# Kernel tuning notes

Measured on AMD Instinct MI355X. Metric: run time of the kernel, lower is better.

The kernel has to match this reference:

```python
import jax, jax.numpy as jnp
import numpy as np

B, S = 16384, 2048
EPS = 1e-8


def _autocorr(x, lag):
    # Pearson correlation between x[:, :-lag] and x[:, lag:] (ddof cancels).
    a = x[:, :-lag]
    b = x[:, lag:]
    am = a.mean(axis=1, keepdims=True)
    bm = b.mean(axis=1, keepdims=True)
    cov = ((a - am) * (b - bm)).mean(axis=1)
    return cov / (a.std(axis=1) * b.std(axis=1))


def _stat_features(x):
    S_len = x.shape[1]
    mean = x.mean(axis=1)
    xc = x - mean[:, None]
    m2 = (xc ** 2).mean(axis=1)
    m3 = (xc ** 3).mean(axis=1)
    m4 = (xc ** 4).mean(axis=1)
    std = jnp.sqrt(m2)
    min_v = x.min(axis=1)
    max_v = x.max(axis=1)
    q = jnp.percentile(x, jnp.array([25.0, 50.0, 75.0]), axis=1)  # [3, B]
    p25, median, p75 = q[0], q[1], q[2]
    diff = jnp.diff(x, axis=1)
    std_diff = diff.std(axis=1)
    trend = std_diff / (std + EPS)
    ac1 = _autocorr(x, 1)
    ac7 = _autocorr(x, 7)
    ac24 = _autocorr(x, 24)
    cv = std / (jnp.abs(mean) + EPS)
    iqr = p75 - p25
    seasonal = x[:, ::24].var(axis=1) / (m2 + EPS)
    skew = m3 / (m2 ** 1.5)          # scipy.stats.skew, bias=True
    kurt = m4 / (m2 ** 2) - 3.0      # scipy.stats.kurtosis, Fisher, bias=True
    length = jnp.full_like(mean, float(S_len))
    sum_abs_diff = jnp.abs(diff).sum(axis=1)
    mean_abs_diff = jnp.abs(diff).mean(axis=1)
    feats = jnp.stack([mean, std, min_v, max_v, median, trend, ac1, ac7, ac24,
                       cv, iqr, seasonal, skew, kurt, length,
                       sum_abs_diff, mean_abs_diff, std_diff, p25, p75], axis=1)
    return jnp.where(jnp.isfinite(feats), feats, 0.0)


def setup_inputs() -> dict:
    key = jax.random.key(0)
    k0, k1, k2, k3, k4 = jax.random.split(key, 5)
    x = jax.random.normal(k0, (B, S), dtype=jnp.float32)
    W1 = jax.random.normal(k1, (64, 20), dtype=jnp.float32) * 0.1
    b1 = jnp.zeros((64,), dtype=jnp.float32)
    W2 = jax.random.normal(k3, (128, 64), dtype=jnp.float32) * 0.1
    b2 = jnp.zeros((128,), dtype=jnp.float32)
    return {"x": x, "W1": W1, "b1": b1, "W2": W2, "b2": b2}


def reference(x, W1, b1, W2, b2):
    feats = _stat_features(x)                      # [B, 20]
    h = jax.nn.relu(feats @ W1.T + b1)             # [B, 64] (dropout inactive at eval)
    return h @ W2.T + b2                           # [B, 128]
```

## Files before the change

kernel.cpp:

```cpp
#include <hip/hip_runtime.h>
#include <cmath>

constexpr int S_LEN = 2048;
constexpr float EPS = 1e-8f;

typedef unsigned uvec32 __attribute__((ext_vector_type(32)));

__device__ __forceinline__ float fin(float v) { return isfinite(v) ? v : 0.0f; }

__device__ __forceinline__ unsigned f2o_bits(unsigned u) {
    return (u & 0x80000000u) ? ~u : (u | 0x80000000u);
}
__device__ __forceinline__ float o2f(unsigned u) {
    return __uint_as_float((u & 0x80000000u) ? (u ^ 0x80000000u) : ~u);
}

template <int Ctrl, int Rmask>
__device__ __forceinline__ int dpp_zero_i(int x) {
    return __builtin_amdgcn_update_dpp(0, x, Ctrl, Rmask, 0xF, true);
}
template <int Ctrl>
__device__ __forceinline__ int dpp_keep_i(int x) {
    return __builtin_amdgcn_update_dpp(x, x, Ctrl, 0xF, 0xF, false);
}
__device__ __forceinline__ int wred_add_i(int v) {
    v += dpp_zero_i<0xB1, 0xF>(v);
    v += dpp_zero_i<0x4E, 0xF>(v);
    v += dpp_zero_i<0x114, 0xF>(v);
    v += dpp_zero_i<0x118, 0xF>(v);
    v += dpp_zero_i<0x142, 0xA>(v);
    v += dpp_zero_i<0x143, 0xC>(v);
    return __builtin_amdgcn_readlane(v, 63);
}
__device__ __forceinline__ float wred_add_f(float v) {
    #define ADDF(CT, RM) v += __uint_as_float((unsigned)dpp_zero_i<CT, RM>((int)__float_as_uint(v)))
    ADDF(0xB1, 0xF); ADDF(0x4E, 0xF); ADDF(0x114, 0xF);
    ADDF(0x118, 0xF); ADDF(0x142, 0xA); ADDF(0x143, 0xC);
    #undef ADDF
    return __uint_as_float((unsigned)__builtin_amdgcn_readlane((int)__float_as_uint(v), 63));
}
__device__ __forceinline__ float wred_min_f(float v) {
    #define MINF(CT) v = fminf(v, __uint_as_float((unsigned)dpp_keep_i<CT>((int)__float_as_uint(v))))
    MINF(0xB1); MINF(0x4E); MINF(0x114); MINF(0x118); MINF(0x142); MINF(0x143);
    #undef MINF
    return __uint_as_float((unsigned)__builtin_amdgcn_readlane((int)__float_as_uint(v), 63));
}
__device__ __forceinline__ float wred_max_f(float v) {
    #define MAXF(CT) v = fmaxf(v, __uint_as_float((unsigned)dpp_keep_i<CT>((int)__float_as_uint(v))))
    MAXF(0xB1); MAXF(0x4E); MAXF(0x114); MAXF(0x118); MAXF(0x142); MAXF(0x143);
    #undef MAXF
    return __uint_as_float((unsigned)__builtin_amdgcn_readlane((int)__float_as_uint(v), 63));
}
__device__ __forceinline__ unsigned wred_umin(unsigned v) {
    #define MINU(CT) { unsigned t = (unsigned)dpp_keep_i<CT>((int)v); v = v < t ? v : t; }
    MINU(0xB1) MINU(0x4E) MINU(0x114) MINU(0x118) MINU(0x142) MINU(0x143)
    #undef MINU
    return (unsigned)__builtin_amdgcn_readlane((int)v, 63);
}
__device__ __forceinline__ float readlane_f(float x, int l) {
    return __uint_as_float((unsigned)__builtin_amdgcn_readlane((int)__float_as_uint(x), l));
}

__device__ __forceinline__ void transpose32(uvec32& A) {
    #pragma unroll
    for (int j = 16; j; j >>= 1) {
        unsigned m = (j == 16) ? 0x0000FFFFu : (j == 8) ? 0x00FF00FFu
                   : (j == 4) ? 0x0F0F0F0Fu : (j == 2) ? 0x33333333u : 0x55555555u;
        #pragma unroll
        for (int k = 0; k < 32; k++) {
            if (!(k & j)) {
                unsigned t = (A[k] ^ (A[k | j] >> j)) & m;
                A[k] = A[k] ^ t;
                A[k | j] = A[k | j] ^ (t << j);
            }
        }
    }
}

#define VF(e) __uint_as_float(a[e])


__global__ __launch_bounds__(256) void statspct_kernel(
    const float* __restrict__ x, float* __restrict__ feats, int nrows)
{
    const int gw   = (blockIdx.x * 256 + threadIdx.x) >> 6;
    const int lane = threadIdx.x & 63;
    if (gw >= nrows) return;

    uvec32 a;
    const float* xr = x + (size_t)gw * S_LEN + lane * 32;
    #pragma unroll
    for (int q = 0; q < 8; q++) {
        float4 t = reinterpret_cast<const float4*>(xr)[q];
        a[4 * q + 0] = __float_as_uint(t.x); a[4 * q + 1] = __float_as_uint(t.y);
        a[4 * q + 2] = __float_as_uint(t.z); a[4 * q + 3] = __float_as_uint(t.w);
    }

    float s1 = 0.f, s2 = 0.f, sd2 = 0.f, sad = 0.f;
    float p1 = 0.f, p7 = 0.f, p24 = 0.f, se1 = 0.f, se2 = 0.f;
    float mn = VF(0), mx = VF(0);
    #pragma unroll
    for (int e = 0; e < 32; e++) {
        float val = VF(e);
        s1 += val; s2 = fmaf(val, val, s2);
        mn = fminf(mn, val); mx = fmaxf(mx, val);
    }
    #pragma unroll
    for (int e = 0; e < 31; e++) {
        float d = VF(e + 1) - VF(e);
        sd2 = fmaf(d, d, sd2); sad += fabsf(d);
        p1 = fmaf(VF(e), VF(e + 1), p1);
    }
    #pragma unroll
    for (int e = 0; e < 25; e++) p7 = fmaf(VF(e), VF(e + 7), p7);
    #pragma unroll
    for (int e = 0; e < 8; e++)  p24 = fmaf(VF(e), VF(e + 24), p24);

    const bool notlast = (lane < 63);
    #pragma unroll
    for (int j = 0; j < 24; j++) {
        float nb = __shfl_down(VF(j), 1, 64);
        float g = notlast ? nb : 0.f;
        p24 = fmaf(VF(8 + j), g, p24);
        if (j < 7) p7 = fmaf(VF(25 + j), g, p7);
        if (j == 0 && notlast) {
            float d = nb - VF(31);
            sd2 = fmaf(d, d, sd2); sad += fabsf(d);
            p1 = fmaf(VF(31), nb, p1);
        }
    }
    {
        int r3 = lane % 3;
        float sv = (r3 == 0) ? VF(0) : ((r3 == 1) ? VF(16) : VF(8));
        se1 += sv; se2 = fmaf(sv, sv, se2);
        if (r3 == 0) { se1 += VF(24); se2 = fmaf(VF(24), VF(24), se2); }
    }
    float aa = 0, bb = 0, h7v = 0, hq7v = 0;
    #pragma unroll
    for (int e = 0; e < 24; e++) {
        aa += VF(e); bb = fmaf(VF(e), VF(e), bb);
        if (e == 6) { h7v = aa; hq7v = bb; }
    }
    float cc = 0, dd = 0, t7v = 0, tq7v = 0;
    #pragma unroll
    for (int e = 31; e >= 8; e--) {
        cc += VF(e); dd = fmaf(VF(e), VF(e), dd);
        if (e == 25) { t7v = cc; tq7v = dd; }
    }
    const float h1  = readlane_f(VF(0), 0),   t1  = readlane_f(VF(31), 63);
    const float h7  = readlane_f(h7v, 0),     hq7 = readlane_f(hq7v, 0);
    const float h24 = readlane_f(aa, 0),      hq24 = readlane_f(bb, 0);
    const float t7  = readlane_f(t7v, 63),    tq7 = readlane_f(tq7v, 63);
    const float t24 = readlane_f(cc, 63),     tq24 = readlane_f(dd, 63);
    const float hq1 = h1 * h1, tq1 = t1 * t1;

    float S1  = wred_add_f(s1);
    float mean = S1 * (1.0f / S_LEN);
    float S2  = wred_add_f(s2);
    float SD2 = wred_add_f(sd2);
    float SAD = wred_add_f(sad);
    float P1  = wred_add_f(p1);
    float P7  = wred_add_f(p7);
    float P24 = wred_add_f(p24);
    float SE1 = wred_add_f(se1);
    float SE2 = wred_add_f(se2);
    float MN  = wred_min_f(mn);
    float MX  = wred_max_f(mx);

    float c2 = 0.f, c3 = 0.f, c4 = 0.f;
    #pragma unroll
    for (int e = 0; e < 32; e++) {
        float xc = VF(e) - mean;
        float q = xc * xc;
        c2 += q; c3 = fmaf(q, xc, c3); c4 = fmaf(q, q, c4);
    }
    float C2 = wred_add_f(c2), C3 = wred_add_f(c3), C4 = wred_add_f(c4);

    {
        const float Sf = (float)S_LEN;
        const float nd = Sf - 1.0f;
        float m2v = C2 / Sf, m3v = C3 / Sf, m4v = C4 / Sf;
        float stdv = sqrtf(m2v);
        float dmean = (t1 - h1) / nd;
        float dvar = SD2 / nd - dmean * dmean;
        float std_diff = sqrtf(fmaxf(dvar, 0.f));
        float trend = std_diff / (stdv + EPS);
        float ac[3];
        const float Ls[3] = {1.f, 7.f, 24.f};
        const float Ps[3] = {P1, P7, P24};
        const float hd[3] = {h1, h7, h24},   hqv[3] = {hq1, hq7, hq24};
        const float tl[3] = {t1, t7, t24},   tqv[3] = {tq1, tq7, tq24};
        #pragma unroll
        for (int q = 0; q < 3; q++) {
            float n = Sf - Ls[q];
            float sa = S1 - tl[q], sb = S1 - hd[q];
            float qa = S2 - tqv[q], qb = S2 - hqv[q];
            float am = sa / n, bm = sb / n;
            float cov = Ps[q] / n - am * bm;
            float as_ = sqrtf(fmaxf(qa / n - am * am, 0.f));
            float bs_ = sqrtf(fmaxf(qb / n - bm * bm, 0.f));
            ac[q] = cov / (as_ * bs_);
        }
        float cv = stdv / (fabsf(mean) + EPS);
        float sm = SE1 / 86.f;
        float svar = SE2 / 86.f - sm * sm;
        float seasonal = svar / (m2v + EPS);
        float skew = m3v / (m2v * stdv);
        float kurt = m4v / (m2v * m2v) - 3.f;
        if (lane == 0) {
            float4* fp = (float4*)(feats + (size_t)gw * 20);
            fp[0] = make_float4(fin(mean), fin(stdv), fin(MN), fin(MX));
            fp[1] = make_float4(fin(trend), fin(ac[0]), fin(ac[1]), fin(ac[2]));
            fp[2] = make_float4(fin(cv), fin(seasonal), fin(skew), fin(kurt));
            fp[3] = make_float4(Sf, fin(SAD), fin(SAD / nd), fin(std_diff));
        }
    }

    #pragma unroll
    for (int e = 0; e < 32; e++) a[e] = f2o_bits(a[e]);
    transpose32(a);

    unsigned act0 = ~0u, act1 = ~0u, act2 = ~0u;
    int K0 = 511, K1 = 1023, K2 = 1535;
    unsigned uK0 = 0, uK1 = 0, uK2 = 0;
    #pragma unroll
    for (int b = 31; b >= 0; b--) {
        unsigned mb = a[31 - b];
        unsigned nmb = ~mb;
        unsigned z0 = act0 & nmb, z1 = act1 & nmb, z2 = act2 & nmb;
        int C01 = wred_add_i(__popc(z0) | (__popc(z1) << 16));
        int Cc2 = wred_add_i(__popc(z2));
        int c0 = C01 & 0xFFFF;
        int c1 = (int)((unsigned)C01 >> 16);
        if (K0 < c0)  act0 = z0; else { K0 -= c0;  act0 &= mb; uK0 |= (1u << b); }
        if (K1 < c1)  act1 = z1; else { K1 -= c1;  act1 &= mb; uK1 |= (1u << b); }
        if (K2 < Cc2) act2 = z2; else { K2 -= Cc2; act2 &= mb; uK2 |= (1u << b); }
    }
    int e01 = wred_add_i(__popc(act0) | (__popc(act1) << 16));
    int eq0 = e01 & 0xFFFF, eq1 = (int)((unsigned)e01 >> 16);
    int eq2 = wred_add_i(__popc(act2));

    transpose32(a);
    unsigned m0 = ~0u, m1 = ~0u, m2 = ~0u;
    #pragma unroll
    for (int e = 0; e < 32; e++) {
        unsigned ue = a[e];
        if (ue > uK0) m0 = m0 < ue ? m0 : ue;
        if (ue > uK1) m1 = m1 < ue ? m1 : ue;
        if (ue > uK2) m2 = m2 < ue ? m2 : ue;
    }
    m0 = wred_umin(m0); m1 = wred_umin(m1); m2 = wred_umin(m2);

    float v511 = o2f(uK0), v1023 = o2f(uK1), v1535 = o2f(uK2);
    float v512  = (K0 + 1 < eq0) ? v511  : o2f(m0);
    float v1024 = (K1 + 1 < eq1) ? v1023 : o2f(m1);
    float v1536 = (K2 + 1 < eq2) ? v1535 : o2f(m2);
    float p25 = v511 + 0.75f * (v512 - v511);
    float med = 0.5f * (v1023 + v1024);
    float p75 = v1535 + 0.25f * (v1536 - v1535);
    float iqr = p75 - p25;

    if (lane == 0) {
        float4* fp = (float4*)(feats + (size_t)gw * 20);
        fp[4] = make_float4(fin(med), fin(iqr), fin(p25), fin(p75));
    }
}

__global__ __launch_bounds__(256) void mlp_kernel(
    const float* __restrict__ feats,
    const float* __restrict__ W1, const float* __restrict__ b1,
    const float* __restrict__ W2, const float* __restrict__ b2,
    float* __restrict__ out, int nrows)
{
    __shared__ float w2s[128 * 65];
    __shared__ float w1s[64 * 21];
    __shared__ float hs[4 * 64];

    static const int perm[20] = {0,1,2,3,5,6,7,8,9,11,12,13,14,15,16,17,4,10,18,19};

    const int tid  = threadIdx.x;
    const int lane = tid & 63;
    const int w    = tid >> 6;

    for (int n = tid; n < 64 * 20; n += 256)
        w1s[(n / 20) * 21 + (n % 20)] = W1[(n / 20) * 20 + perm[n % 20]];
    #pragma unroll 8
    for (int it = 0; it < 32; it++) {
        int n = tid + 256 * it;
        w2s[(n >> 6) * 65 + (n & 63)] = W2[n];
    }
    const float b1v = b1[lane];
    const int j  = tid & 127;
    const int r0 = tid >> 7;
    const float b2v = b2[j];
    __syncthreads();

    for (int rg = blockIdx.x * 4; rg < nrows; rg += gridDim.x * 4) {
        {
            int row = min(rg + w, nrows - 1);
            const float* fp = feats + (size_t)row * 20;
            float acc = b1v;
            #pragma unroll
            for (int k = 0; k < 20; k++)
                acc = fmaf(fp[k], w1s[lane * 21 + k], acc);
            hs[w * 64 + lane] = fmaxf(acc, 0.f);
        }
        __syncthreads();
        {
            int r1 = r0 + 2;
            float acc0 = b2v, acc1 = b2v;
            #pragma unroll
            for (int k = 0; k < 64; k++) {
                float wv2 = w2s[j * 65 + k];
                acc0 = fmaf(hs[r0 * 64 + k], wv2, acc0);
                acc1 = fmaf(hs[r1 * 64 + k], wv2, acc1);
            }
            if (rg + r0 < nrows) out[(size_t)(rg + r0) * 128 + j] = acc0;
            if (rg + r1 < nrows) out[(size_t)(rg + r1) * 128 + j] = acc1;
        }
        __syncthreads();
    }
}

extern "C" void kernel_launch(void* const* d_in, const int* in_sizes, int n_in,
                              void* d_out, int out_size, void* d_ws, size_t ws_size,
                              hipStream_t stream) {
    const float* x  = (const float*)d_in[0];
    const float* W1 = (const float*)d_in[1];
    const float* b1 = (const float*)d_in[2];
    const float* W2 = (const float*)d_in[3];
    const float* b2 = (const float*)d_in[4];
    float* out   = (float*)d_out;
    float* feats = (float*)d_ws;
    int nrows = in_sizes[0] / S_LEN;
    int blocks = (nrows + 3) / 4;
    statspct_kernel<<<blocks, 256, 0, stream>>>(x, feats, nrows);
    mlp_kernel<<<512, 256, 0, stream>>>(feats, W1, b1, W2, b2, out, nrows);
}
```

Measured before the change: 281.7 us.

## Fuse MLP into the stats kernel, using pre-transposed weights read from global memory

Removes the separate MLP kernel. Each wavefront keeps its row's 20 features in shared memory and computes both MLP layers itself, reading transposed W1 and W2 that a small pre-kernel writes to the workspace. This drops the feature round-trip through global memory and the second big launch. In exchange, every wave reads the weights from global memory or cache instead of LDS, and an extra tiny launch is added. Synchronisation within the wave relies on s_waitcnt plus a sched_barrier rather than a block barrier.

```diff
diff --git a/kernel.cpp b/kernel.cpp
--- a/kernel.cpp
+++ b/kernel.cpp
@@ -79,12 +79,32 @@
 
 #define VF(e) __uint_as_float(a[e])
 
-
-__global__ __launch_bounds__(256) void statspct_kernel(
-    const float* __restrict__ x, float* __restrict__ feats, int nrows)
+__global__ __launch_bounds__(256) void transpose_w_kernel(
+    const float* __restrict__ W1, const float* __restrict__ W2, float* __restrict__ wt)
 {
+    int tid = blockIdx.x * blockDim.x + threadIdx.x;
+    int stride = gridDim.x * blockDim.x;
+    for (int n = tid; n < 64 * 20; n += stride) {
+        int j = n & 63, k = n >> 6;
+        wt[n] = W1[j * 20 + k];
+    }
+    for (int n = tid; n < 128 * 64; n += stride) {
+        int o = n & 127, k = n >> 7;
+        wt[1280 + n] = W2[o * 64 + k];
+    }
+}
+
+__global__ __launch_bounds__(256) void fused_stats_mlp_kernel(
+    const float* __restrict__ x, const float* __restrict__ wt,
+    const float* __restrict__ b1, const float* __restrict__ b2,
+    float* __restrict__ out, int nrows)
+{
+    __shared__ __align__(16) float sf[4][20];
+    __shared__ __align__(16) float hsh[4][64];
+
     const int gw   = (blockIdx.x * 256 + threadIdx.x) >> 6;
     const int lane = threadIdx.x & 63;
+    const int w    = (threadIdx.x >> 6);
     if (gw >= nrows) return;
 
     uvec32 a;
@@ -208,11 +228,15 @@
         float skew = m3v / (m2v * stdv);
         float kurt = m4v / (m2v * m2v) - 3.f;
         if (lane == 0) {
-            float4* fp = (float4*)(feats + (size_t)gw * 20);
-            fp[0] = make_float4(fin(mean), fin(stdv), fin(MN), fin(MX));
-            fp[1] = make_float4(fin(trend), fin(ac[0]), fin(ac[1]), fin(ac[2]));
-            fp[2] = make_float4(fin(cv), fin(seasonal), fin(skew), fin(kurt));
-            fp[3] = make_float4(Sf, fin(SAD), fin(SAD / nd), fin(std_diff));
+            float* s = sf[w];
+            s[0]  = fin(mean);     s[1]  = fin(stdv);
+            s[2]  = fin(MN);       s[3]  = fin(MX);
+            s[5]  = fin(trend);    s[6]  = fin(ac[0]);
+            s[7]  = fin(ac[1]);    s[8]  = fin(ac[2]);
+            s[9]  = fin(cv);       s[11] = fin(seasonal);
+            s[12] = fin(skew);     s[13] = fin(kurt);
+            s[14] = Sf;            s[15] = fin(SAD);
+            s[16] = fin(SAD / nd); s[17] = fin(std_diff);
         }
     }
 
@@ -261,65 +285,61 @@
     float iqr = p75 - p25;
 
     if (lane == 0) {
-        float4* fp = (float4*)(feats + (size_t)gw * 20);
-        fp[4] = make_float4(fin(med), fin(iqr), fin(p25), fin(p75));
-    }
-}
-
-__global__ __launch_bounds__(256) void mlp_kernel(
-    const float* __restrict__ feats,
-    const float* __restrict__ W1, const float* __restrict__ b1,
-    const float* __restrict__ W2, const float* __restrict__ b2,
-    float* __restrict__ out, int nrows)
-{
-    __shared__ float w2s[128 * 65];
-    __shared__ float w1s[64 * 21];
-    __shared__ float hs[4 * 64];
-
-    static const int perm[20] = {0,1,2,3,5,6,7,8,9,11,12,13,14,15,16,17,4,10,18,19};
-
-    const int tid  = threadIdx.x;
-    const int lane = tid & 63;
-    const int w    = tid >> 6;
-
-    for (int n = tid; n < 64 * 20; n += 256)
-        w1s[(n / 20) * 21 + (n % 20)] = W1[(n / 20) * 20 + perm[n % 20]];
-    #pragma unroll 8
-    for (int it = 0; it < 32; it++) {
-        int n = tid + 256 * it;
-        w2s[(n >> 6) * 65 + (n & 63)] = W2[n];
-    }
-    const float b1v = b1[lane];
-    const int j  = tid & 127;
-    const int r0 = tid >> 7;
-    const float b2v = b2[j];
-    __syncthreads();
-
-    for (int rg = blockIdx.x * 4; rg < nrows; rg += gridDim.x * 4) {
-        {
-            int row = min(rg + w, nrows - 1);
-            const float* fp = feats + (size_t)row * 20;
-            float acc = b1v;
-            #pragma unroll
-            for (int k = 0; k < 20; k++)
-                acc = fmaf(fp[k], w1s[lane * 21 + k], acc);
-            hs[w * 64 + lane] = fmaxf(acc, 0.f);
-        }
-        __syncthreads();
-        {
-            int r1 = r0 + 2;
-            float acc0 = b2v, acc1 = b2v;
-            #pragma unroll
-            for (int k = 0; k < 64; k++) {
-                float wv2 = w2s[j * 65 + k];
-                acc0 = fmaf(hs[r0 * 64 + k], wv2, acc0);
-                acc1 = fmaf(hs[r1 * 64 + k], wv2, acc1);
-            }
-            if (rg + r0 < nrows) out[(size_t)(rg + r0) * 128 + j] = acc0;
-            if (rg + r1 < nrows) out[(size_t)(rg + r1) * 128 + j] = acc1;
-        }
-        __syncthreads();
-    }
+        float* s = sf[w];
+        s[4]  = fin(med); s[10] = fin(iqr);
+        s[18] = fin(p25); s[19] = fin(p75);
+    }
+    __asm__ volatile("s_waitcnt lgkmcnt(0)" ::: "memory");
+    __builtin_amdgcn_sched_barrier(0);
+
+    const float* W1T = wt;
+    const float* W2T = wt + 1280;
+    const float4* sfv = (const float4*)sf[w];
+    float4 f0 = sfv[0], f1 = sfv[1], f2 = sfv[2], f3 = sfv[3], f4 = sfv[4];
+    float h = b1[lane];
+    h = fmaf(f0.x, W1T[ 0 * 64 + lane], h);
+    h = fmaf(f0.y, W1T[ 1 * 64 + lane], h);
+    h = fmaf(f0.z, W1T[ 2 * 64 + lane], h);
+    h = fmaf(f0.w, W1T[ 3 * 64 + lane], h);
+    h = fmaf(f1.x, W1T[ 4 * 64 + lane], h);
+    h = fmaf(f1.y, W1T[ 5 * 64 + lane], h);
+    h = fmaf(f1.z, W1T[ 6 * 64 + lane], h);
+    h = fmaf(f1.w, W1T[ 7 * 64 + lane], h);
+    h = fmaf(f2.x, W1T[ 8 * 64 + lane], h);
+    h = fmaf(f2.y, W1T[ 9 * 64 + lane], h);
+    h = fmaf(f2.z, W1T[10 * 64 + lane], h);
+    h = fmaf(f2.w, W1T[11 * 64 + lane], h);
+    h = fmaf(f3.x, W1T[12 * 64 + lane], h);
+    h = fmaf(f3.y, W1T[13 * 64 + lane], h);
+    h = fmaf(f3.z, W1T[14 * 64 + lane], h);
+    h = fmaf(f3.w, W1T[15 * 64 + lane], h);
+    h = fmaf(f4.x, W1T[16 * 64 + lane], h);
+    h = fmaf(f4.y, W1T[17 * 64 + lane], h);
+    h = fmaf(f4.z, W1T[18 * 64 + lane], h);
+    h = fmaf(f4.w, W1T[19 * 64 + lane], h);
+    h = fmaxf(h, 0.f);
+    hsh[w][lane] = h;
+    __asm__ volatile("s_waitcnt lgkmcnt(0)" ::: "memory");
+    __builtin_amdgcn_sched_barrier(0);
+
+    const int j2 = lane * 2;
+    float2 b2v = *(const float2*)(b2 + j2);
+    float acc0 = b2v.x, acc1 = b2v.y;
+    const float4* hv4 = (const float4*)hsh[w];
+    #pragma unroll
+    for (int q = 0; q < 16; q++) {
+        float4 hq = hv4[q];
+        const float* wp = W2T + (4 * q) * 128 + j2;
+        float2 w0 = *(const float2*)(wp);
+        float2 w1 = *(const float2*)(wp + 128);
+        float2 w2 = *(const float2*)(wp + 256);
+        float2 w3 = *(const float2*)(wp + 384);
+        acc0 = fmaf(hq.x, w0.x, acc0); acc1 = fmaf(hq.x, w0.y, acc1);
+        acc0 = fmaf(hq.y, w1.x, acc0); acc1 = fmaf(hq.y, w1.y, acc1);
+        acc0 = fmaf(hq.z, w2.x, acc0); acc1 = fmaf(hq.z, w2.y, acc1);
+        acc0 = fmaf(hq.w, w3.x, acc0); acc1 = fmaf(hq.w, w3.y, acc1);
+    }
+    *(float2*)(out + (size_t)gw * 128 + j2) = make_float2(acc0, acc1);
 }
 
 extern "C" void kernel_launch(void* const* d_in, const int* in_sizes, int n_in,
@@ -330,10 +350,10 @@
     const float* b1 = (const float*)d_in[2];
     const float* W2 = (const float*)d_in[3];
     const float* b2 = (const float*)d_in[4];
-    float* out   = (float*)d_out;
-    float* feats = (float*)d_ws;
+    float* out = (float*)d_out;
+    float* wt  = (float*)d_ws;
     int nrows = in_sizes[0] / S_LEN;
     int blocks = (nrows + 3) / 4;
-    statspct_kernel<<<blocks, 256, 0, stream>>>(x, feats, nrows);
-    mlp_kernel<<<512, 256, 0, stream>>>(feats, W1, b1, W2, b2, out, nrows);
-}
+    transpose_w_kernel<<<8, 256, 0, stream>>>(W1, W2, wt);
+    fused_stats_mlp_kernel<<<blocks, 256, 0, stream>>>(x, wt, b1, b2, out, nrows);
+}
```

New measurement: 274.5 us. 1.03x faster.
